# Kernel optimization log

Measured on AMD Instinct MI355X. Metric: run time of the kernel, lower is better.

## Reference

```python
import jax, jax.numpy as jnp
import numpy as np

TOP_K = 2
EPS = 1e-8

def setup_inputs() -> dict:
    key = jax.random.key(0)
    k1, k2 = jax.random.split(key)
    T, D, E = 16384, 4096, 128  # tokens, d_model, num_experts
    x = jax.random.normal(k1, (T, D), dtype=jnp.float32)
    W = jax.random.normal(k2, (E, D), dtype=jnp.float32) * (1.0 / np.sqrt(D))
    b = jnp.zeros((E,), dtype=jnp.float32)
    return {"x": x, "W": W, "b": b}

def reference(x, W, b):
    # gate linear: [T, D] @ [D, E] -> [T, E]
    logits = jnp.einsum('td,ed->te', x, W) + b
    probs = jax.nn.softmax(logits, axis=-1)
    top_k_probs, top_k_indices = jax.lax.top_k(probs, TOP_K)
    top_k_probs = top_k_probs / (jnp.sum(top_k_probs, axis=-1, keepdims=True) + EPS)
    return (top_k_indices, top_k_probs)
```

## Files before the change

kernel.cpp:

```cpp
#include <hip/hip_runtime.h>
#include <math.h>


#define T_TOKENS 16384
#define D_K      4096
#define N_EXP    128
#define TOK_BLK  64
#define KSTEP    64
#define NITER    (D_K / KSTEP)

typedef float  f32x4  __attribute__((ext_vector_type(4)));
typedef short  bf16x8 __attribute__((ext_vector_type(8)));
typedef float  fragc  __attribute__((ext_vector_type(4)));

__device__ __forceinline__ unsigned short bf16_rne(float f) {
    unsigned u = __float_as_uint(f);
    u += 0x7FFFu + ((u >> 16) & 1u);
    return (unsigned short)(u >> 16);
}
__device__ __forceinline__ float bf16f(unsigned short h) {
    return __uint_as_float(((unsigned)h) << 16);
}

__device__ __forceinline__ int a_off(int G, int l) {
    const int L  = G * 64 + l;
    const int sw = ((L >> 3) ^ G) & 7;
    return (L << 4) ^ (sw << 4);
}

__global__ __launch_bounds__(256)
void prep_w(const float* __restrict__ W,
            short* __restrict__ wh, short* __restrict__ wl) {
    const int gid = blockIdx.x * 256 + threadIdx.x;
    const int l   = gid & 63;
    const int ntk = gid >> 6;
    const int e   = ((ntk & 7) << 4) + (l & 15);
    const int k   = ((ntk >> 3) << 5) + ((l >> 4) << 3);
    const float* src = W + (size_t)e * D_K + k;
    const f32x4 v0 = *(const f32x4*)src;
    const f32x4 v1 = *(const f32x4*)(src + 4);
    bf16x8 hv, lv;
#pragma unroll
    for (int j = 0; j < 8; ++j) {
        const float f = (j < 4) ? v0[j] : v1[j - 4];
        const unsigned short hh = bf16_rne(f);
        hv[j] = (short)hh;
        lv[j] = (short)bf16_rne(f - bf16f(hh));
    }
    *(bf16x8*)(wh + (size_t)gid * 8) = hv;
    *(bf16x8*)(wl + (size_t)gid * 8) = lv;
}

#define LOGSTRIDE 140
#define MERGE_OFF (64 * LOGSTRIDE * 4)
#define SMEM_SZ   (MERGE_OFF + 64 * 4 * 8 * 4)

__global__ __launch_bounds__(256, 1)
void router_mfma(const float* __restrict__ x,
                 const short* __restrict__ wh,
                 const short* __restrict__ wl,
                 const float* __restrict__ bvec,
                 float* __restrict__ out) {
    __shared__ __align__(16) char smem[SMEM_SZ];

    const int tid  = threadIdx.x;
    const int lane = tid & 63;
    const int w    = tid >> 6;
    const int wm   = w >> 1;
    const int wn   = w & 1;
    const int g    = blockIdx.x;

    const int s_tok = tid >> 3;
    const int s_kc8 = tid & 7;
    const float* xsrc = x + (size_t)(g * TOK_BLK + s_tok) * D_K + s_kc8 * 8;
    const int kb_s = s_kc8 >> 2;
    const int l_s  = (s_tok & 15) | ((s_kc8 & 3) << 4);

    f32x4 ld[4];
    auto issue = [&](int t) {
        const float* p = xsrc + t * KSTEP;
        ld[0] = *(const f32x4*)p;
        ld[1] = *(const f32x4*)(p + 4);
        ld[2] = *(const f32x4*)(p + (size_t)32 * D_K);
        ld[3] = *(const f32x4*)(p + (size_t)32 * D_K + 4);
    };
    auto commit = [&](int bufbase) {
#pragma unroll
        for (int r = 0; r < 2; ++r) {
            const int tokL = s_tok + 32 * r;
            const int G    = kb_s * 4 + (tokL >> 4);
            const int off  = a_off(G, l_s);
            bf16x8 hv, lv;
#pragma unroll
            for (int j = 0; j < 8; ++j) {
                const float f = (j < 4) ? ld[2 * r][j] : ld[2 * r + 1][j - 4];
                const unsigned short hh = bf16_rne(f);
                hv[j] = (short)hh;
                lv[j] = (short)bf16_rne(f - bf16f(hh));
            }
            *(bf16x8*)(smem + bufbase + off)        = hv;
            *(bf16x8*)(smem + bufbase + 8192 + off) = lv;
        }
    };

    fragc acc[2][4];
#pragma unroll
    for (int mi = 0; mi < 2; ++mi)
#pragma unroll
        for (int nt = 0; nt < 4; ++nt)
            acc[mi][nt] = (fragc){0.f, 0.f, 0.f, 0.f};

    issue(0);
    commit(0);
    issue(1);
    __syncthreads();

    for (int t = 0; t < NITER; ++t) {
        const int cur = (t & 1) << 14;
#pragma unroll
        for (int kb = 0; kb < 2; ++kb) {
            const int kbG = t * 2 + kb;
            bf16x8 bh[4], bl[4], ah[2], al[2];
#pragma unroll
            for (int nt = 0; nt < 4; ++nt) {
                const size_t line = ((size_t)(kbG * 8 + wn * 4 + nt)) * 64 + lane;
                bh[nt] = *(const bf16x8*)(wh + line * 8);
                bl[nt] = *(const bf16x8*)(wl + line * 8);
            }
#pragma unroll
            for (int mi = 0; mi < 2; ++mi) {
                const int G   = kb * 4 + wm * 2 + mi;
                const int off = a_off(G, lane);
                ah[mi] = *(const bf16x8*)(smem + cur + off);
                al[mi] = *(const bf16x8*)(smem + cur + 8192 + off);
            }
#pragma unroll
            for (int mi = 0; mi < 2; ++mi)
#pragma unroll
                for (int nt = 0; nt < 4; ++nt) {
                    acc[mi][nt] = __builtin_amdgcn_mfma_f32_16x16x32_bf16(
                        ah[mi], bh[nt], acc[mi][nt], 0, 0, 0);
                    acc[mi][nt] = __builtin_amdgcn_mfma_f32_16x16x32_bf16(
                        al[mi], bh[nt], acc[mi][nt], 0, 0, 0);
                    acc[mi][nt] = __builtin_amdgcn_mfma_f32_16x16x32_bf16(
                        ah[mi], bl[nt], acc[mi][nt], 0, 0, 0);
                }
        }
        if (t + 1 < NITER) {
            commit(16384 - cur);
            if (t + 2 < NITER) issue(t + 2);
        }
        __syncthreads();
    }

    float* lg = (float*)smem;
#pragma unroll
    for (int mi = 0; mi < 2; ++mi) {
        const int row0 = (wm * 2 + mi) * 16 + ((lane >> 4) << 2);
#pragma unroll
        for (int nt = 0; nt < 4; ++nt) {
            const int col = wn * 64 + nt * 16 + (lane & 15);
#pragma unroll
            for (int j = 0; j < 4; ++j)
                lg[(row0 + j) * LOGSTRIDE + col] = acc[mi][nt][j];
        }
    }
    __syncthreads();

    const int tok = tid & 63;
    const int q   = tid >> 6;
    const float* lrow = lg + tok * LOGSTRIDE + q * 32;
    const float* brow = bvec + q * 32;
    float v1 = -INFINITY, v2 = -INFINITY;
    int   i1 = 0, i2 = 0;
#pragma unroll 8
    for (int c = 0; c < 32; ++c) {
        const float lv = lrow[c] + brow[c];
        if (lv > v1)      { v2 = v1; i2 = i1; v1 = lv; i1 = c; }
        else if (lv > v2) { v2 = lv; i2 = c; }
    }
    float Z = 0.f;
#pragma unroll 8
    for (int c = 0; c < 32; ++c) Z += expf(lrow[c] + brow[c] - v1);

    float* mrow = (float*)(smem + MERGE_OFF) + (tok * 4 + q) * 8;
    mrow[0] = v1; mrow[1] = (float)(q * 32 + i1);
    mrow[2] = v2; mrow[3] = (float)(q * 32 + i2);
    mrow[4] = Z;
    __syncthreads();

    if (tid < 64) {
        const float* m0 = (float*)(smem + MERGE_OFF) + tid * 32;
        float V1 = m0[0], I1 = m0[1], V2 = m0[2], I2 = m0[3], Zs = m0[4];
#pragma unroll
        for (int q2 = 1; q2 < 4; ++q2) {
            const float* mq = m0 + q2 * 8;
            const float a1 = mq[0], ai1 = mq[1], a2 = mq[2], ai2 = mq[3], Zq = mq[4];
            const float M  = fmaxf(V1, a1);
            Zs = Zs * expf(V1 - M) + Zq * expf(a1 - M);
            if (a1 > V1)      { V2 = V1; I2 = I1; V1 = a1; I1 = ai1; }
            else if (a1 > V2) { V2 = a1; I2 = ai1; }
            if (a2 > V2)      { V2 = a2; I2 = ai2; }
        }
        const float p1 = 1.0f / Zs;
        const float p2 = expf(V2 - V1) / Zs;
        const float s  = p1 + p2 + 1e-8f;
        const int tokG = g * TOK_BLK + tid;
        float2* oidx  = (float2*)out;
        float2* oprob = ((float2*)out) + T_TOKENS;
        oidx[tokG]  = make_float2(I1, I2);
        oprob[tokG] = make_float2(p1 / s, p2 / s);
    }
}

extern "C" void kernel_launch(void* const* d_in, const int* in_sizes, int n_in,
                              void* d_out, int out_size, void* d_ws, size_t ws_size,
                              hipStream_t stream) {
    (void)in_sizes; (void)n_in; (void)out_size; (void)ws_size;
    const float* x = (const float*)d_in[0];
    const float* W = (const float*)d_in[1];
    const float* b = (const float*)d_in[2];
    float* out = (float*)d_out;
    short* wh = (short*)d_ws;
    short* wl = (short*)d_ws + (size_t)N_EXP * D_K;

    prep_w<<<dim3(256), dim3(256), 0, stream>>>(W, wh, wl);
    router_mfma<<<dim3(T_TOKENS / TOK_BLK), dim3(256), 0, stream>>>(x, wh, wl, b, out);
}
```

Before: 407.8 us.

## Use 512-thread blocks with 8 waves splitting experts and move staging before MFMA

Doubles the block to 8 waves (2x4 over tokens by experts), so each wave computes a 32x32 tile and each thread stages half as much x data. The next tile's convert-and-store to LDS now happens before the current tile's MFMAs, and all B fragments for the step are loaded up front. Launch bounds now allow two blocks per CU. The top-2/softmax reduction is split 8 ways with a padded merge buffer. The goal is more latency hiding and occupancy, at the cost of more waves reloading the same W fragments from global memory.

```diff
diff --git a/kernel.cpp b/kernel.cpp
--- a/kernel.cpp
+++ b/kernel.cpp
@@ -53,9 +53,9 @@
 
 #define LOGSTRIDE 140
 #define MERGE_OFF (64 * LOGSTRIDE * 4)
-#define SMEM_SZ   (MERGE_OFF + 64 * 4 * 8 * 4)
-
-__global__ __launch_bounds__(256, 1)
+#define SMEM_SZ   (MERGE_OFF + 64 * 8 * 9 * 4)
+
+__global__ __launch_bounds__(512, 2)
 void router_mfma(const float* __restrict__ x,
                  const short* __restrict__ wh,
                  const short* __restrict__ wl,
@@ -66,48 +66,44 @@
     const int tid  = threadIdx.x;
     const int lane = tid & 63;
     const int w    = tid >> 6;
-    const int wm   = w >> 1;
-    const int wn   = w & 1;
+    const int wm   = w >> 2;
+    const int wn   = w & 3;
     const int g    = blockIdx.x;
 
     const int s_tok = tid >> 3;
     const int s_kc8 = tid & 7;
     const float* xsrc = x + (size_t)(g * TOK_BLK + s_tok) * D_K + s_kc8 * 8;
-    const int kb_s = s_kc8 >> 2;
-    const int l_s  = (s_tok & 15) | ((s_kc8 & 3) << 4);
-
-    f32x4 ld[4];
+    const int G_s   = ((s_kc8 >> 2) << 2) + (s_tok >> 4);
+    const int l_s   = (s_tok & 15) | ((s_kc8 & 3) << 4);
+    const int off_s = a_off(G_s, l_s);
+
+    f32x4 ld0, ld1;
     auto issue = [&](int t) {
-        const float* p = xsrc + t * KSTEP;
-        ld[0] = *(const f32x4*)p;
-        ld[1] = *(const f32x4*)(p + 4);
-        ld[2] = *(const f32x4*)(p + (size_t)32 * D_K);
-        ld[3] = *(const f32x4*)(p + (size_t)32 * D_K + 4);
+        const float* p = xsrc + (size_t)t * KSTEP;
+        ld0 = *(const f32x4*)p;
+        ld1 = *(const f32x4*)(p + 4);
     };
     auto commit = [&](int bufbase) {
-#pragma unroll
-        for (int r = 0; r < 2; ++r) {
-            const int tokL = s_tok + 32 * r;
-            const int G    = kb_s * 4 + (tokL >> 4);
-            const int off  = a_off(G, l_s);
-            bf16x8 hv, lv;
-#pragma unroll
-            for (int j = 0; j < 8; ++j) {
-                const float f = (j < 4) ? ld[2 * r][j] : ld[2 * r + 1][j - 4];
-                const unsigned short hh = bf16_rne(f);
-                hv[j] = (short)hh;
-                lv[j] = (short)bf16_rne(f - bf16f(hh));
-            }
-            *(bf16x8*)(smem + bufbase + off)        = hv;
-            *(bf16x8*)(smem + bufbase + 8192 + off) = lv;
-        }
+        bf16x8 hv, lv;
+#pragma unroll
+        for (int j = 0; j < 8; ++j) {
+            const float f = (j < 4) ? ld0[j] : ld1[j - 4];
+            const unsigned short hh = bf16_rne(f);
+            hv[j] = (short)hh;
+            lv[j] = (short)bf16_rne(f - bf16f(hh));
+        }
+        *(bf16x8*)(smem + bufbase + off_s)        = hv;
+        *(bf16x8*)(smem + bufbase + 8192 + off_s) = lv;
     };
 
-    fragc acc[2][4];
+    const short* base_h = wh + ((size_t)(wn * 2) * 64 + lane) * 8;
+    const short* base_l = wl + ((size_t)(wn * 2) * 64 + lane) * 8;
+
+    fragc acc[2][2];
 #pragma unroll
     for (int mi = 0; mi < 2; ++mi)
 #pragma unroll
-        for (int nt = 0; nt < 4; ++nt)
+        for (int nt = 0; nt < 2; ++nt)
             acc[mi][nt] = (fragc){0.f, 0.f, 0.f, 0.f};
 
     issue(0);
@@ -117,49 +113,54 @@
 
     for (int t = 0; t < NITER; ++t) {
         const int cur = (t & 1) << 14;
+
+        if (t + 1 < NITER) {
+            commit(cur ^ (1 << 14));
+            if (t + 2 < NITER) issue(t + 2);
+        }
+
+        bf16x8 bh[2][2], bl[2][2];
 #pragma unroll
         for (int kb = 0; kb < 2; ++kb) {
-            const int kbG = t * 2 + kb;
-            bf16x8 bh[4], bl[4], ah[2], al[2];
-#pragma unroll
-            for (int nt = 0; nt < 4; ++nt) {
-                const size_t line = ((size_t)(kbG * 8 + wn * 4 + nt)) * 64 + lane;
-                bh[nt] = *(const bf16x8*)(wh + line * 8);
-                bl[nt] = *(const bf16x8*)(wl + line * 8);
+            const size_t kofs = (size_t)(2 * t + kb) * 4096;
+#pragma unroll
+            for (int nt = 0; nt < 2; ++nt) {
+                bh[kb][nt] = *(const bf16x8*)(base_h + kofs + nt * 512);
+                bl[kb][nt] = *(const bf16x8*)(base_l + kofs + nt * 512);
             }
+        }
+
+#pragma unroll
+        for (int kb = 0; kb < 2; ++kb) {
+            bf16x8 ah[2], al[2];
 #pragma unroll
             for (int mi = 0; mi < 2; ++mi) {
-                const int G   = kb * 4 + wm * 2 + mi;
-                const int off = a_off(G, lane);
+                const int off = a_off(kb * 4 + wm * 2 + mi, lane);
                 ah[mi] = *(const bf16x8*)(smem + cur + off);
                 al[mi] = *(const bf16x8*)(smem + cur + 8192 + off);
             }
 #pragma unroll
             for (int mi = 0; mi < 2; ++mi)
 #pragma unroll
-                for (int nt = 0; nt < 4; ++nt) {
+                for (int nt = 0; nt < 2; ++nt) {
                     acc[mi][nt] = __builtin_amdgcn_mfma_f32_16x16x32_bf16(
-                        ah[mi], bh[nt], acc[mi][nt], 0, 0, 0);
+                        ah[mi], bh[kb][nt], acc[mi][nt], 0, 0, 0);
                     acc[mi][nt] = __builtin_amdgcn_mfma_f32_16x16x32_bf16(
-                        al[mi], bh[nt], acc[mi][nt], 0, 0, 0);
+                        al[mi], bh[kb][nt], acc[mi][nt], 0, 0, 0);
                     acc[mi][nt] = __builtin_amdgcn_mfma_f32_16x16x32_bf16(
-                        ah[mi], bl[nt], acc[mi][nt], 0, 0, 0);
+                        ah[mi], bl[kb][nt], acc[mi][nt], 0, 0, 0);
                 }
         }
-        if (t + 1 < NITER) {
-            commit(16384 - cur);
-            if (t + 2 < NITER) issue(t + 2);
-        }
         __syncthreads();
     }
 
     float* lg = (float*)smem;
 #pragma unroll
     for (int mi = 0; mi < 2; ++mi) {
-        const int row0 = (wm * 2 + mi) * 16 + ((lane >> 4) << 2);
-#pragma unroll
-        for (int nt = 0; nt < 4; ++nt) {
-            const int col = wn * 64 + nt * 16 + (lane & 15);
+        const int row0 = wm * 32 + mi * 16 + ((lane >> 4) << 2);
+#pragma unroll
+        for (int nt = 0; nt < 2; ++nt) {
+            const int col = wn * 32 + nt * 16 + (lane & 15);
 #pragma unroll
             for (int j = 0; j < 4; ++j)
                 lg[(row0 + j) * LOGSTRIDE + col] = acc[mi][nt][j];
@@ -169,32 +170,32 @@
 
     const int tok = tid & 63;
     const int q   = tid >> 6;
-    const float* lrow = lg + tok * LOGSTRIDE + q * 32;
-    const float* brow = bvec + q * 32;
+    const float* lrow = lg + tok * LOGSTRIDE + q * 16;
+    const float* brow = bvec + q * 16;
     float v1 = -INFINITY, v2 = -INFINITY;
     int   i1 = 0, i2 = 0;
-#pragma unroll 8
-    for (int c = 0; c < 32; ++c) {
+#pragma unroll
+    for (int c = 0; c < 16; ++c) {
         const float lv = lrow[c] + brow[c];
         if (lv > v1)      { v2 = v1; i2 = i1; v1 = lv; i1 = c; }
         else if (lv > v2) { v2 = lv; i2 = c; }
     }
     float Z = 0.f;
-#pragma unroll 8
-    for (int c = 0; c < 32; ++c) Z += expf(lrow[c] + brow[c] - v1);
-
-    float* mrow = (float*)(smem + MERGE_OFF) + (tok * 4 + q) * 8;
-    mrow[0] = v1; mrow[1] = (float)(q * 32 + i1);
-    mrow[2] = v2; mrow[3] = (float)(q * 32 + i2);
+#pragma unroll
+    for (int c = 0; c < 16; ++c) Z += expf(lrow[c] + brow[c] - v1);
+
+    float* mrow = (float*)(smem + MERGE_OFF) + (tok * 8 + q) * 9;
+    mrow[0] = v1; mrow[1] = (float)(q * 16 + i1);
+    mrow[2] = v2; mrow[3] = (float)(q * 16 + i2);
     mrow[4] = Z;
     __syncthreads();
 
     if (tid < 64) {
-        const float* m0 = (float*)(smem + MERGE_OFF) + tid * 32;
+        const float* m0 = (float*)(smem + MERGE_OFF) + tid * 72;
         float V1 = m0[0], I1 = m0[1], V2 = m0[2], I2 = m0[3], Zs = m0[4];
 #pragma unroll
-        for (int q2 = 1; q2 < 4; ++q2) {
-            const float* mq = m0 + q2 * 8;
+        for (int q2 = 1; q2 < 8; ++q2) {
+            const float* mq = m0 + q2 * 9;
             const float a1 = mq[0], ai1 = mq[1], a2 = mq[2], ai2 = mq[3], Zq = mq[4];
             const float M  = fmaxf(V1, a1);
             Zs = Zs * expf(V1 - M) + Zq * expf(a1 - M);
@@ -225,5 +226,5 @@
     short* wl = (short*)d_ws + (size_t)N_EXP * D_K;
 
     prep_w<<<dim3(256), dim3(256), 0, stream>>>(W, wh, wl);
-    router_mfma<<<dim3(T_TOKENS / TOK_BLK), dim3(256), 0, stream>>>(x, wh, wl, b, out);
-}
+    router_mfma<<<dim3(T_TOKENS / TOK_BLK), dim3(512), 0, stream>>>(x, wh, wl, b, out);
+}
```

New measurement: 421.3 us. +3.3%, slower.
